# Kernel optimization log

Measured on AMD Instinct MI355X. Metric: run time of the kernel, lower is better.

The kernel has to match this reference:

```python
import jax, jax.numpy as jnp
import numpy as np

N = 12                      # matrix size (input_size)
TRI = N * (N + 1) // 2      # 78 lower-triangular entries
HID = 512
BATCH = 262144


def setup_inputs() -> dict:
    key = jax.random.key(0)
    ks = jax.random.split(key, 4)
    s1 = 1.0 / np.sqrt(N)
    s2 = 1.0 / np.sqrt(HID)
    return {
        "x": jax.random.normal(ks[0], (BATCH, N), dtype=jnp.float32),
        "W1": jax.random.normal(ks[1], (N, HID), dtype=jnp.float32) * s1,
        "b1": jnp.zeros((HID,), dtype=jnp.float32),
        "W2": jax.random.normal(ks[2], (HID, HID), dtype=jnp.float32) * s2,
        "b2": jnp.zeros((HID,), dtype=jnp.float32),
        "W3": jax.random.normal(ks[3], (HID, TRI + 1), dtype=jnp.float32) * s2,
        "b3": jnp.zeros((TRI + 1,), dtype=jnp.float32),
    }


def reference(x, W1, b1, W2, b2, W3, b3):
    # 3-layer MLP (assumed parent-class structure): relu, relu, softplus
    h = jax.nn.relu(x @ W1 + b1)
    h = jax.nn.relu(h @ W2 + b2)
    out = jax.nn.softplus(h @ W3 + b3)          # [B, TRI+1]
    # Vectorized row-major lower-triangular scatter (replaces nested python loop)
    rows, cols = jnp.tril_indices(N)            # row-major order matches idx loop
    B = x.shape[0]
    L = jnp.zeros((B, N, N), dtype=out.dtype).at[:, rows, cols].set(out[:, :TRI])
    MMT = jnp.einsum('bij,bkj->bik', L, L)      # M @ M^T, PSD [B, N, N]
    c = out[:, TRI]                             # [B]
    return MMT, c
```

## Files before the change

### kernel.cpp

```cpp
#include <hip/hip_runtime.h>
#include <math.h>

typedef __attribute__((ext_vector_type(8))) _Float16 fp16x8;
typedef __attribute__((ext_vector_type(4))) _Float16 fp16x4;
typedef __attribute__((ext_vector_type(4))) float floatx4;

#define HID 512
#define TRIC 78
#define OUTC 79
#define BATCH 262144
#define HPAD 520
#define OPAD 84
#define XPAD 24
#define X_OFF 33280

#define W2P_OFF 16384
#define W3P_OFF 278528

__global__ __launch_bounds__(256) void prep_kernel(const float* __restrict__ W1,
                                                   const float* __restrict__ W2,
                                                   const float* __restrict__ W3,
                                                   _Float16* __restrict__ wsh) {
  int g = blockIdx.x * 256 + threadIdx.x;
  int lane = g & 63;
  int l15 = lane & 15, q = lane >> 4;
  fp16x8 v;
  if (g < 2048) {
    int ct = g >> 6;
    int c = ct * 16 + l15;
#pragma unroll
    for (int j = 0; j < 8; ++j) {
      int k = q * 8 + j;
      v[j] = (k < 12) ? (_Float16)W1[k * HID + c] : (_Float16)0.f;
    }
    *(fp16x8*)(wsh + (size_t)g * 8) = v;
  } else if (g < 34816) {
    int h = g - 2048;
    int fk = h >> 6;
    int kb = fk & 15, ct = fk >> 4;
    int c = ct * 16 + l15;
    int kbase = kb * 32 + q * 8;
#pragma unroll
    for (int j = 0; j < 8; ++j) v[j] = (_Float16)W2[(kbase + j) * HID + c];
    *(fp16x8*)(wsh + W2P_OFF + (size_t)h * 8) = v;
  } else if (g < 39936) {
    int h = g - 34816;
    int fk = h >> 6;
    int kb = fk & 15, ct = fk >> 4;
    int c = ct * 16 + l15;
    int kbase = kb * 32 + q * 8;
#pragma unroll
    for (int j = 0; j < 8; ++j)
      v[j] = (c < OUTC) ? (_Float16)W3[(kbase + j) * OUTC + c] : (_Float16)0.f;
    *(fp16x8*)(wsh + W3P_OFF + (size_t)h * 8) = v;
  }
}

__device__ __forceinline__ float softplus_f(float v) {
  float e = __expf(-fabsf(v));
  return fmaxf(v, 0.f) + __logf(1.f + e);
}

__global__ __launch_bounds__(512, 4) void fused_kernel(const float* __restrict__ x,
                                                       const float* __restrict__ b1,
                                                       const float* __restrict__ b2,
                                                       const float* __restrict__ b3,
                                                       const _Float16* __restrict__ wsh,
                                                       float* __restrict__ out) {
  __shared__ __align__(16) _Float16 hbuf[X_OFF + 64 * XPAD];
  const int tid = threadIdx.x;
  const int wave = tid >> 6, lane = tid & 63;
  const int l15 = lane & 15, quad = lane >> 4;
  const int r0 = blockIdx.x * 64;

  const fp16x8* w1p = (const fp16x8*)wsh;
  const fp16x8* w2p = (const fp16x8*)(wsh + W2P_OFF);
  const fp16x8* w3p = (const fp16x8*)(wsh + W3P_OFF);

  {
    _Float16* xs = hbuf + X_OFF;
    const float* xg = x + (size_t)r0 * 12;
    if (tid < 256) {
      int e = 512 + tid;
      int row = e / 12, col = e - row * 12;
      xs[row * XPAD + col] = (_Float16)xg[e];
      xs[(tid >> 2) * XPAD + 12 + (tid & 3)] = (_Float16)0.f;
    }
    {
      int row = tid / 12, col = tid - row * 12;
      xs[row * XPAD + col] = (_Float16)xg[tid];
    }
  }
  fp16x8 a1p[4];
#pragma unroll
  for (int ct = 0; ct < 4; ++ct) a1p[ct] = w1p[(wave * 4 + ct) * 64 + lane];
  __syncthreads();

  fp16x8 zf;
#pragma unroll
  for (int j = 0; j < 8; ++j) zf[j] = (_Float16)0.f;

  floatx4 bq[4];
#pragma unroll
  for (int ct = 0; ct < 4; ++ct)
    bq[ct] = *(const floatx4*)(b1 + wave * 64 + ct * 16 + quad * 4);

  floatx4 acc[4][4];
#pragma unroll
  for (int ct = 0; ct < 4; ++ct)
#pragma unroll
    for (int nt = 0; nt < 4; ++nt) acc[ct][nt] = bq[ct];

  {
    const _Float16* xs = hbuf + X_OFF;
    fp16x8 xb[4];
#pragma unroll
    for (int nt = 0; nt < 4; ++nt)
      xb[nt] = (quad < 2) ? *(const fp16x8*)(xs + (nt * 16 + l15) * XPAD + quad * 8) : zf;
#pragma unroll
    for (int ct = 0; ct < 4; ++ct) {
#pragma unroll
      for (int nt = 0; nt < 4; ++nt)
        acc[ct][nt] = __builtin_amdgcn_mfma_f32_16x16x32_f16(a1p[ct], xb[nt], acc[ct][nt], 0, 0, 0);
    }
  }

#pragma unroll
  for (int ct = 0; ct < 4; ++ct)
#pragma unroll
    for (int nt = 0; nt < 4; ++nt) {
      fp16x4 p;
#pragma unroll
      for (int r = 0; r < 4; ++r) p[r] = (_Float16)fmaxf(acc[ct][nt][r], 0.f);
      *(fp16x4*)(hbuf + (nt * 16 + l15) * HPAD + wave * 64 + ct * 16 + quad * 4) = p;
    }
  fp16x8 ap[4];
#pragma unroll
  for (int ct = 0; ct < 4; ++ct) ap[ct] = w2p[((wave * 4 + ct) * 16 + 0) * 64 + lane];
  __syncthreads();

#pragma unroll
  for (int ct = 0; ct < 4; ++ct)
    bq[ct] = *(const floatx4*)(b2 + wave * 64 + ct * 16 + quad * 4);
#pragma unroll
  for (int ct = 0; ct < 4; ++ct)
#pragma unroll
    for (int nt = 0; nt < 4; ++nt) acc[ct][nt] = bq[ct];

#pragma unroll 2
  for (int kb = 0; kb < 16; ++kb) {
    fp16x8 a[4], b[4];
#pragma unroll
    for (int ct = 0; ct < 4; ++ct) a[ct] = ap[ct];
#pragma unroll
    for (int nt = 0; nt < 4; ++nt)
      b[nt] = *(const fp16x8*)(hbuf + (nt * 16 + l15) * HPAD + kb * 32 + quad * 8);
    const int kbn = (kb + 1) & 15;
#pragma unroll
    for (int ct = 0; ct < 4; ++ct) ap[ct] = w2p[((wave * 4 + ct) * 16 + kbn) * 64 + lane];
    __builtin_amdgcn_s_setprio(1);
#pragma unroll
    for (int ct = 0; ct < 4; ++ct)
#pragma unroll
      for (int nt = 0; nt < 4; ++nt)
        acc[ct][nt] = __builtin_amdgcn_mfma_f32_16x16x32_f16(a[ct], b[nt], acc[ct][nt], 0, 0, 0);
    __builtin_amdgcn_s_setprio(0);
  }

  __syncthreads();

#pragma unroll
  for (int ct = 0; ct < 4; ++ct)
#pragma unroll
    for (int nt = 0; nt < 4; ++nt) {
      fp16x4 p;
#pragma unroll
      for (int r = 0; r < 4; ++r) p[r] = (_Float16)fmaxf(acc[ct][nt][r], 0.f);
      *(fp16x4*)(hbuf + (nt * 16 + l15) * HPAD + wave * 64 + ct * 16 + quad * 4) = p;
    }

  const int mt3 = wave >> 1;
  const int codd = wave & 1;
  const int c0 = codd ? 3 : 0;
  const int nct = codd ? 2 : 3;

  floatx4 b3q[3];
#pragma unroll
  for (int j = 0; j < 3; ++j) {
#pragma unroll
    for (int r = 0; r < 4; ++r) {
      int c = (c0 + j) * 16 + quad * 4 + r;
      b3q[j][r] = (j < nct && c < OUTC) ? b3[c] : 0.f;
    }
  }
  floatx4 acc3[3];
#pragma unroll
  for (int j = 0; j < 3; ++j) acc3[j] = b3q[j];

  fp16x8 ap3[3];
#pragma unroll
  for (int j = 0; j < 3; ++j) ap3[j] = zf;
#pragma unroll
  for (int j = 0; j < 3; ++j)
    if (j < nct) ap3[j] = w3p[((c0 + j) * 16 + 0) * 64 + lane];
  __syncthreads();

#pragma unroll 2
  for (int kb = 0; kb < 16; ++kb) {
    fp16x8 bfrag = *(const fp16x8*)(hbuf + (mt3 * 16 + l15) * HPAD + kb * 32 + quad * 8);
    fp16x8 a3[3];
#pragma unroll
    for (int j = 0; j < 3; ++j) a3[j] = ap3[j];
    const int kbn = (kb + 1) & 15;
#pragma unroll
    for (int j = 0; j < 3; ++j)
      if (j < nct) ap3[j] = w3p[((c0 + j) * 16 + kbn) * 64 + lane];
    __builtin_amdgcn_s_setprio(1);
#pragma unroll
    for (int j = 0; j < 3; ++j)
      if (j < nct)
        acc3[j] = __builtin_amdgcn_mfma_f32_16x16x32_f16(a3[j], bfrag, acc3[j], 0, 0, 0);
    __builtin_amdgcn_s_setprio(0);
  }
  __syncthreads();

  float* outf = (float*)hbuf;
#pragma unroll
  for (int j = 0; j < 3; ++j)
    if (j < nct) {
      floatx4 v;
#pragma unroll
      for (int r = 0; r < 4; ++r) v[r] = softplus_f(acc3[j][r]);
      *(floatx4*)(outf + (mt3 * 16 + l15) * OPAD + (c0 + j) * 16 + quad * 4) = v;
    }
  if (codd && quad == 3)
    out[(size_t)BATCH * 144 + r0 + mt3 * 16 + l15] = softplus_f(acc3[1][2]);
  __syncthreads();

  {
    const float* Lbase = (const float*)hbuf;
    const int rowl = tid >> 3;
    const int sub = tid & 7;
    const float* Lr = Lbase + rowl * OPAD;

    float R[80];
#pragma unroll
    for (int q = 0; q < 20; ++q) {
      floatx4 v = *(const floatx4*)(Lr + q * 4);
#pragma unroll
      for (int r = 0; r < 4; ++r) R[q * 4 + r] = v[r];
    }

    float Lj0[12], Lj1[12];
    {
      const int tj = (sub * (sub + 1)) >> 1;
#pragma unroll
      for (int k = 0; k < 12; ++k) Lj0[k] = (k <= sub) ? Lr[tj + k] : 0.f;
#pragma unroll
      for (int k = 0; k < 12; ++k) Lj1[k] = 0.f;
      const int j1 = sub + 8;
      if (sub < 4) {
        const int tj1 = (j1 * (j1 + 1)) >> 1;
#pragma unroll
        for (int k = 0; k < 12; ++k) Lj1[k] = (k <= j1) ? Lr[tj1 + k] : 0.f;
      }
    }

    float* Mg = out + ((size_t)r0 + rowl) * 144;
#pragma unroll
    for (int i = 0; i < 12; ++i) {
      const int ti = (i * (i + 1)) >> 1;
      float s0 = 0.f, s1 = 0.f;
#pragma unroll
      for (int k = 0; k <= i; ++k) {
        const float li = R[ti + k];
        s0 = fmaf(li, Lj0[k], s0);
        s1 = fmaf(li, Lj1[k], s1);
      }
      Mg[i * 12 + sub] = s0;
      if (sub < 4) Mg[i * 12 + sub + 8] = s1;
    }
  }
}

extern "C" void kernel_launch(void* const* d_in, const int* in_sizes, int n_in,
                              void* d_out, int out_size, void* d_ws, size_t ws_size,
                              hipStream_t stream) {
  const float* x  = (const float*)d_in[0];
  const float* W1 = (const float*)d_in[1];
  const float* b1 = (const float*)d_in[2];
  const float* W2 = (const float*)d_in[3];
  const float* b2 = (const float*)d_in[4];
  const float* W3 = (const float*)d_in[5];
  const float* b3 = (const float*)d_in[6];
  float* out = (float*)d_out;
  _Float16* wsh = (_Float16*)d_ws;

  prep_kernel<<<156, 256, 0, stream>>>(W1, W2, W3, wsh);
  fused_kernel<<<BATCH / 64, 512, 0, stream>>>(x, b1, b2, b3, wsh, out);
}
```

Measured before the change: 329.6 us.

## Load x directly to registers and double-buffer weight prefetch two k-steps ahead

The input rows are now read straight from global memory into MFMA B-fragments, so the LDS staging area for x and one barrier are gone, which also shrinks the shared-memory footprint. The layer-2 and layer-3 weight fragment prefetch becomes two-deep (ping-pong buffers loaded two k-blocks ahead) with the k loops fully unrolled, to hide global/L2 latency behind MFMAs. The cost is more VGPRs under the 512-thread, 4-blocks launch bound, which risks spills, plus a longer unrolled code body.

```diff
diff --git a/kernel.cpp b/kernel.cpp
--- a/kernel.cpp
+++ b/kernel.cpp
@@ -11,8 +11,6 @@
 #define BATCH 262144
 #define HPAD 520
 #define OPAD 84
-#define XPAD 24
-#define X_OFF 33280
 
 #define W2P_OFF 16384
 #define W3P_OFF 278528
@@ -67,7 +65,7 @@
                                                        const float* __restrict__ b3,
                                                        const _Float16* __restrict__ wsh,
                                                        float* __restrict__ out) {
-  __shared__ __align__(16) _Float16 hbuf[X_OFF + 64 * XPAD];
+  __shared__ __align__(16) _Float16 hbuf[64 * HPAD];
   const int tid = threadIdx.x;
   const int wave = tid >> 6, lane = tid & 63;
   const int l15 = lane & 15, quad = lane >> 4;
@@ -77,29 +75,28 @@
   const fp16x8* w2p = (const fp16x8*)(wsh + W2P_OFF);
   const fp16x8* w3p = (const fp16x8*)(wsh + W3P_OFF);
 
-  {
-    _Float16* xs = hbuf + X_OFF;
-    const float* xg = x + (size_t)r0 * 12;
-    if (tid < 256) {
-      int e = 512 + tid;
-      int row = e / 12, col = e - row * 12;
-      xs[row * XPAD + col] = (_Float16)xg[e];
-      xs[(tid >> 2) * XPAD + 12 + (tid & 3)] = (_Float16)0.f;
-    }
-    {
-      int row = tid / 12, col = tid - row * 12;
-      xs[row * XPAD + col] = (_Float16)xg[tid];
-    }
-  }
-  fp16x8 a1p[4];
-#pragma unroll
-  for (int ct = 0; ct < 4; ++ct) a1p[ct] = w1p[(wave * 4 + ct) * 64 + lane];
-  __syncthreads();
-
   fp16x8 zf;
 #pragma unroll
   for (int j = 0; j < 8; ++j) zf[j] = (_Float16)0.f;
 
+  fp16x8 xb[4];
+#pragma unroll
+  for (int nt = 0; nt < 4; ++nt) {
+    const float* p = x + ((size_t)r0 + nt * 16 + l15) * 12;
+    fp16x8 v = zf;
+    if (quad == 0) {
+      floatx4 u0 = *(const floatx4*)(p);
+      floatx4 u1 = *(const floatx4*)(p + 4);
+#pragma unroll
+      for (int j = 0; j < 4; ++j) { v[j] = (_Float16)u0[j]; v[4 + j] = (_Float16)u1[j]; }
+    } else if (quad == 1) {
+      floatx4 u2 = *(const floatx4*)(p + 8);
+#pragma unroll
+      for (int j = 0; j < 4; ++j) v[j] = (_Float16)u2[j];
+    }
+    xb[nt] = v;
+  }
+
   floatx4 bq[4];
 #pragma unroll
   for (int ct = 0; ct < 4; ++ct)
@@ -111,18 +108,12 @@
 #pragma unroll
     for (int nt = 0; nt < 4; ++nt) acc[ct][nt] = bq[ct];
 
-  {
-    const _Float16* xs = hbuf + X_OFF;
-    fp16x8 xb[4];
+#pragma unroll
+  for (int ct = 0; ct < 4; ++ct) {
+    fp16x8 a1 = w1p[(wave * 4 + ct) * 64 + lane];
 #pragma unroll
     for (int nt = 0; nt < 4; ++nt)
-      xb[nt] = (quad < 2) ? *(const fp16x8*)(xs + (nt * 16 + l15) * XPAD + quad * 8) : zf;
-#pragma unroll
-    for (int ct = 0; ct < 4; ++ct) {
-#pragma unroll
-      for (int nt = 0; nt < 4; ++nt)
-        acc[ct][nt] = __builtin_amdgcn_mfma_f32_16x16x32_f16(a1p[ct], xb[nt], acc[ct][nt], 0, 0, 0);
-    }
+      acc[ct][nt] = __builtin_amdgcn_mfma_f32_16x16x32_f16(a1, xb[nt], acc[ct][nt], 0, 0, 0);
   }
 
 #pragma unroll
@@ -134,10 +125,12 @@
       for (int r = 0; r < 4; ++r) p[r] = (_Float16)fmaxf(acc[ct][nt][r], 0.f);
       *(fp16x4*)(hbuf + (nt * 16 + l15) * HPAD + wave * 64 + ct * 16 + quad * 4) = p;
     }
-  fp16x8 ap[4];
-#pragma unroll
-  for (int ct = 0; ct < 4; ++ct) ap[ct] = w2p[((wave * 4 + ct) * 16 + 0) * 64 + lane];
-  __syncthreads();
+  fp16x8 ap[2][4];
+#pragma unroll
+  for (int ct = 0; ct < 4; ++ct) ap[0][ct] = w2p[((wave * 4 + ct) * 16 + 0) * 64 + lane];
+  __syncthreads();
+#pragma unroll
+  for (int ct = 0; ct < 4; ++ct) ap[1][ct] = w2p[((wave * 4 + ct) * 16 + 1) * 64 + lane];
 
 #pragma unroll
   for (int ct = 0; ct < 4; ++ct)
@@ -147,17 +140,20 @@
 #pragma unroll
     for (int nt = 0; nt < 4; ++nt) acc[ct][nt] = bq[ct];
 
-#pragma unroll 2
+#pragma unroll
   for (int kb = 0; kb < 16; ++kb) {
+    const int par = kb & 1;
     fp16x8 a[4], b[4];
 #pragma unroll
-    for (int ct = 0; ct < 4; ++ct) a[ct] = ap[ct];
+    for (int ct = 0; ct < 4; ++ct) a[ct] = ap[par][ct];
 #pragma unroll
     for (int nt = 0; nt < 4; ++nt)
       b[nt] = *(const fp16x8*)(hbuf + (nt * 16 + l15) * HPAD + kb * 32 + quad * 8);
-    const int kbn = (kb + 1) & 15;
-#pragma unroll
-    for (int ct = 0; ct < 4; ++ct) ap[ct] = w2p[((wave * 4 + ct) * 16 + kbn) * 64 + lane];
+    if (kb < 14) {
+#pragma unroll
+      for (int ct = 0; ct < 4; ++ct)
+        ap[par][ct] = w2p[((wave * 4 + ct) * 16 + kb + 2) * 64 + lane];
+    }
     __builtin_amdgcn_s_setprio(1);
 #pragma unroll
     for (int ct = 0; ct < 4; ++ct)
@@ -197,24 +193,29 @@
 #pragma unroll
   for (int j = 0; j < 3; ++j) acc3[j] = b3q[j];
 
-  fp16x8 ap3[3];
-#pragma unroll
-  for (int j = 0; j < 3; ++j) ap3[j] = zf;
+  fp16x8 ap3[2][3];
+#pragma unroll
+  for (int j = 0; j < 3; ++j) { ap3[0][j] = zf; ap3[1][j] = zf; }
 #pragma unroll
   for (int j = 0; j < 3; ++j)
-    if (j < nct) ap3[j] = w3p[((c0 + j) * 16 + 0) * 64 + lane];
-  __syncthreads();
-
-#pragma unroll 2
+    if (j < nct) ap3[0][j] = w3p[((c0 + j) * 16 + 0) * 64 + lane];
+  __syncthreads();
+#pragma unroll
+  for (int j = 0; j < 3; ++j)
+    if (j < nct) ap3[1][j] = w3p[((c0 + j) * 16 + 1) * 64 + lane];
+
+#pragma unroll
   for (int kb = 0; kb < 16; ++kb) {
+    const int par = kb & 1;
     fp16x8 bfrag = *(const fp16x8*)(hbuf + (mt3 * 16 + l15) * HPAD + kb * 32 + quad * 8);
     fp16x8 a3[3];
 #pragma unroll
-    for (int j = 0; j < 3; ++j) a3[j] = ap3[j];
-    const int kbn = (kb + 1) & 15;
-#pragma unroll
-    for (int j = 0; j < 3; ++j)
-      if (j < nct) ap3[j] = w3p[((c0 + j) * 16 + kbn) * 64 + lane];
+    for (int j = 0; j < 3; ++j) a3[j] = ap3[par][j];
+    if (kb < 14) {
+#pragma unroll
+      for (int j = 0; j < 3; ++j)
+        if (j < nct) ap3[par][j] = w3p[((c0 + j) * 16 + kb + 2) * 64 + lane];
+    }
     __builtin_amdgcn_s_setprio(1);
 #pragma unroll
     for (int j = 0; j < 3; ++j)
```

Result: slower. 702.1 us (+113.0%).

## Halve rows per block to 32 with 4 waves each covering 128 hidden columns

Applied to the files above, without the earlier changes.

Each block now handles 32 batch rows with 256 threads instead of 64 rows with 512 threads. Each wave computes 8 column tiles by 2 row tiles, rather than 4 by 4, in layers 1 and 2. Per-iteration weight prefetches are moved to sit right after each MFMA to shorten register lifetimes and overlap loads with compute. Each W2/W3 fragment fetched from global memory now serves half as many rows, which doubles weight traffic per row. The hope is that smaller blocks and less LDS per block give better occupancy and scheduling.

```diff
diff --git a/kernel.cpp b/kernel.cpp
--- a/kernel.cpp
+++ b/kernel.cpp
@@ -9,10 +9,11 @@
 #define TRIC 78
 #define OUTC 79
 #define BATCH 262144
+#define ROWS 32
 #define HPAD 520
 #define OPAD 84
 #define XPAD 24
-#define X_OFF 33280
+#define X_OFF 16640
 
 #define W2P_OFF 16384
 #define W3P_OFF 278528
@@ -61,17 +62,17 @@
   return fmaxf(v, 0.f) + __logf(1.f + e);
 }
 
-__global__ __launch_bounds__(512, 4) void fused_kernel(const float* __restrict__ x,
+__global__ __launch_bounds__(256, 4) void fused_kernel(const float* __restrict__ x,
                                                        const float* __restrict__ b1,
                                                        const float* __restrict__ b2,
                                                        const float* __restrict__ b3,
                                                        const _Float16* __restrict__ wsh,
                                                        float* __restrict__ out) {
-  __shared__ __align__(16) _Float16 hbuf[X_OFF + 64 * XPAD];
+  __shared__ __align__(16) _Float16 hbuf[X_OFF + ROWS * XPAD];
   const int tid = threadIdx.x;
   const int wave = tid >> 6, lane = tid & 63;
   const int l15 = lane & 15, quad = lane >> 4;
-  const int r0 = blockIdx.x * 64;
+  const int r0 = blockIdx.x * ROWS;
 
   const fp16x8* w1p = (const fp16x8*)wsh;
   const fp16x8* w2p = (const fp16x8*)(wsh + W2P_OFF);
@@ -80,103 +81,96 @@
   {
     _Float16* xs = hbuf + X_OFF;
     const float* xg = x + (size_t)r0 * 12;
-    if (tid < 256) {
-      int e = 512 + tid;
-      int row = e / 12, col = e - row * 12;
-      xs[row * XPAD + col] = (_Float16)xg[e];
-      xs[(tid >> 2) * XPAD + 12 + (tid & 3)] = (_Float16)0.f;
-    }
     {
       int row = tid / 12, col = tid - row * 12;
       xs[row * XPAD + col] = (_Float16)xg[tid];
     }
-  }
-  fp16x8 a1p[4];
-#pragma unroll
-  for (int ct = 0; ct < 4; ++ct) a1p[ct] = w1p[(wave * 4 + ct) * 64 + lane];
+    if (tid < 128) {
+      int e2 = 256 + tid;
+      int r2 = e2 / 12, c2 = e2 - r2 * 12;
+      xs[r2 * XPAD + c2] = (_Float16)xg[e2];
+      xs[(tid >> 2) * XPAD + 12 + (tid & 3)] = (_Float16)0.f;
+    }
+  }
   __syncthreads();
 
   fp16x8 zf;
 #pragma unroll
   for (int j = 0; j < 8; ++j) zf[j] = (_Float16)0.f;
 
-  floatx4 bq[4];
-#pragma unroll
-  for (int ct = 0; ct < 4; ++ct)
-    bq[ct] = *(const floatx4*)(b1 + wave * 64 + ct * 16 + quad * 4);
-
-  floatx4 acc[4][4];
-#pragma unroll
-  for (int ct = 0; ct < 4; ++ct)
-#pragma unroll
-    for (int nt = 0; nt < 4; ++nt) acc[ct][nt] = bq[ct];
+  floatx4 acc[8][2];
+#pragma unroll
+  for (int ct = 0; ct < 8; ++ct) {
+    floatx4 bqc = *(const floatx4*)(b1 + wave * 128 + ct * 16 + quad * 4);
+#pragma unroll
+    for (int nt = 0; nt < 2; ++nt) acc[ct][nt] = bqc;
+  }
 
   {
     const _Float16* xs = hbuf + X_OFF;
-    fp16x8 xb[4];
-#pragma unroll
-    for (int nt = 0; nt < 4; ++nt)
+    fp16x8 xb[2];
+#pragma unroll
+    for (int nt = 0; nt < 2; ++nt)
       xb[nt] = (quad < 2) ? *(const fp16x8*)(xs + (nt * 16 + l15) * XPAD + quad * 8) : zf;
 #pragma unroll
-    for (int ct = 0; ct < 4; ++ct) {
-#pragma unroll
-      for (int nt = 0; nt < 4; ++nt)
-        acc[ct][nt] = __builtin_amdgcn_mfma_f32_16x16x32_f16(a1p[ct], xb[nt], acc[ct][nt], 0, 0, 0);
-    }
-  }
-
-#pragma unroll
-  for (int ct = 0; ct < 4; ++ct)
-#pragma unroll
-    for (int nt = 0; nt < 4; ++nt) {
+    for (int ct = 0; ct < 8; ++ct) {
+      fp16x8 a1 = w1p[(wave * 8 + ct) * 64 + lane];
+#pragma unroll
+      for (int nt = 0; nt < 2; ++nt)
+        acc[ct][nt] = __builtin_amdgcn_mfma_f32_16x16x32_f16(a1, xb[nt], acc[ct][nt], 0, 0, 0);
+    }
+  }
+
+#pragma unroll
+  for (int ct = 0; ct < 8; ++ct)
+#pragma unroll
+    for (int nt = 0; nt < 2; ++nt) {
       fp16x4 p;
 #pragma unroll
       for (int r = 0; r < 4; ++r) p[r] = (_Float16)fmaxf(acc[ct][nt][r], 0.f);
-      *(fp16x4*)(hbuf + (nt * 16 + l15) * HPAD + wave * 64 + ct * 16 + quad * 4) = p;
-    }
-  fp16x8 ap[4];
-#pragma unroll
-  for (int ct = 0; ct < 4; ++ct) ap[ct] = w2p[((wave * 4 + ct) * 16 + 0) * 64 + lane];
-  __syncthreads();
-
-#pragma unroll
-  for (int ct = 0; ct < 4; ++ct)
-    bq[ct] = *(const floatx4*)(b2 + wave * 64 + ct * 16 + quad * 4);
-#pragma unroll
-  for (int ct = 0; ct < 4; ++ct)
-#pragma unroll
-    for (int nt = 0; nt < 4; ++nt) acc[ct][nt] = bq[ct];
+      *(fp16x4*)(hbuf + (nt * 16 + l15) * HPAD + wave * 128 + ct * 16 + quad * 4) = p;
+    }
+  fp16x8 ap[8];
+#pragma unroll
+  for (int ct = 0; ct < 8; ++ct) ap[ct] = w2p[((wave * 8 + ct) * 16 + 0) * 64 + lane];
+  __syncthreads();
+
+#pragma unroll
+  for (int ct = 0; ct < 8; ++ct) {
+    floatx4 bqc = *(const floatx4*)(b2 + wave * 128 + ct * 16 + quad * 4);
+    floatx4 a0 = acc[ct][0], a1v = acc[ct][1];
+    (void)a0; (void)a1v;
+#pragma unroll
+    for (int nt = 0; nt < 2; ++nt) acc[ct][nt] = bqc;
+  }
 
 #pragma unroll 2
   for (int kb = 0; kb < 16; ++kb) {
-    fp16x8 a[4], b[4];
-#pragma unroll
-    for (int ct = 0; ct < 4; ++ct) a[ct] = ap[ct];
-#pragma unroll
-    for (int nt = 0; nt < 4; ++nt)
+    fp16x8 b[2];
+#pragma unroll
+    for (int nt = 0; nt < 2; ++nt)
       b[nt] = *(const fp16x8*)(hbuf + (nt * 16 + l15) * HPAD + kb * 32 + quad * 8);
     const int kbn = (kb + 1) & 15;
-#pragma unroll
-    for (int ct = 0; ct < 4; ++ct) ap[ct] = w2p[((wave * 4 + ct) * 16 + kbn) * 64 + lane];
     __builtin_amdgcn_s_setprio(1);
 #pragma unroll
-    for (int ct = 0; ct < 4; ++ct)
-#pragma unroll
-      for (int nt = 0; nt < 4; ++nt)
-        acc[ct][nt] = __builtin_amdgcn_mfma_f32_16x16x32_f16(a[ct], b[nt], acc[ct][nt], 0, 0, 0);
+    for (int ct = 0; ct < 8; ++ct) {
+      acc[ct][0] = __builtin_amdgcn_mfma_f32_16x16x32_f16(ap[ct], b[0], acc[ct][0], 0, 0, 0);
+      acc[ct][1] = __builtin_amdgcn_mfma_f32_16x16x32_f16(ap[ct], b[1], acc[ct][1], 0, 0, 0);
+      ap[ct] = w2p[((wave * 8 + ct) * 16 + kbn) * 64 + lane];
+    }
     __builtin_amdgcn_s_setprio(0);
   }
 
   __syncthreads();
 
 #pragma unroll
-  for (int ct = 0; ct < 4; ++ct)
-#pragma unroll
-    for (int nt = 0; nt < 4; ++nt) {
+  for (int ct = 0; ct < 8; ++ct)
+#pragma unroll
+    for (int nt = 0; nt < 2; ++nt) {
       fp16x4 p;
 #pragma unroll
       for (int r = 0; r < 4; ++r) p[r] = (_Float16)fmaxf(acc[ct][nt][r], 0.f);
-      *(fp16x4*)(hbuf + (nt * 16 + l15) * HPAD + wave * 64 + ct * 16 + quad * 4) = p;
+      *(fp16x4*)(hbuf + (nt * 16 + l15) * HPAD + wave * 128 + ct * 16 + quad * 4) = p;
     }
 
   const int mt3 = wave >> 1;
@@ -208,18 +202,14 @@
 #pragma unroll 2
   for (int kb = 0; kb < 16; ++kb) {
     fp16x8 bfrag = *(const fp16x8*)(hbuf + (mt3 * 16 + l15) * HPAD + kb * 32 + quad * 8);
-    fp16x8 a3[3];
-#pragma unroll
-    for (int j = 0; j < 3; ++j) a3[j] = ap3[j];
     const int kbn = (kb + 1) & 15;
+    __builtin_amdgcn_s_setprio(1);
 #pragma unroll
     for (int j = 0; j < 3; ++j)
-      if (j < nct) ap3[j] = w3p[((c0 + j) * 16 + kbn) * 64 + lane];
-    __builtin_amdgcn_s_setprio(1);
-#pragma unroll
-    for (int j = 0; j < 3; ++j)
-      if (j < nct)
-        acc3[j] = __builtin_amdgcn_mfma_f32_16x16x32_f16(a3[j], bfrag, acc3[j], 0, 0, 0);
+      if (j < nct) {
+        acc3[j] = __builtin_amdgcn_mfma_f32_16x16x32_f16(ap3[j], bfrag, acc3[j], 0, 0, 0);
+        ap3[j] = w3p[((c0 + j) * 16 + kbn) * 64 + lane];
+      }
     __builtin_amdgcn_s_setprio(0);
   }
   __syncthreads();
@@ -297,5 +287,5 @@
   _Float16* wsh = (_Float16*)d_ws;
 
   prep_kernel<<<156, 256, 0, stream>>>(W1, W2, W3, wsh);
-  fused_kernel<<<BATCH / 64, 512, 0, stream>>>(x, b1, b2, b3, wsh, out);
-}
+  fused_kernel<<<BATCH / ROWS, 256, 0, stream>>>(x, b1, b2, b3, wsh, out);
+}
```

Result: slower. 386.0 us (+17.1%).
